# Kernel optimization log

Measured on AMD Instinct MI355X. Metric: run time of the kernel, lower is better.

Reference implementation:

```python
import jax, jax.numpy as jnp
import numpy as np

B, L, H, NH, DH = 2, 4096, 768, 12, 64
W_ = 128          # one-sided sliding window
NL = 2            # encoder layers
VOCAB, OUT, FF = 50265, 384, 3072
EPS = 1e-5


def _ln(x, s, b):
    m = jnp.mean(x, axis=-1, keepdims=True)
    v = jnp.mean((x - m) ** 2, axis=-1, keepdims=True)
    return (x - m) / jnp.sqrt(v + EPS) * s + b


def _attn(x, amask, Wq, bq, Wk, bk, Wv, bv, Wo, bo):
    # x: [B,L,H]; sliding-window attention (one-sided W_) + global token 0
    def heads(Wt, bt):
        return (x @ Wt + bt).reshape(B, L, NH, DH).transpose(0, 2, 1, 3)  # [B,NH,L,DH]
    q, k, v = heads(Wq, bq), heads(Wk, bk), heads(Wv, bv)
    scale = 1.0 / np.sqrt(DH).astype(np.float32)
    C = W_
    nC = L // C
    qc = q.reshape(B, NH, nC, C, DH)

    def blocks(t):  # gather [prev, self, next] key chunks -> [B,NH,nC,3C,DH]
        tc = t.reshape(B, NH, nC, C, DH)
        tp = jnp.pad(tc, ((0, 0), (0, 0), (1, 1), (0, 0), (0, 0)))
        return jnp.concatenate([tp[:, :, :-2], tp[:, :, 1:-1], tp[:, :, 2:]], axis=3)

    k3, v3 = blocks(k), blocks(v)
    s_loc = jnp.einsum('bhncd,bhnkd->bhnck', qc, k3) * scale  # [B,NH,nC,C,3C]

    pos_k = (jnp.arange(nC)[:, None] - 1) * C + jnp.arange(3 * C)[None, :]  # [nC,3C]
    pos_q = jnp.arange(nC)[:, None] * C + jnp.arange(C)[None, :]            # [nC,C]
    within = jnp.abs(pos_q[:, :, None] - pos_k[:, None, :]) <= W_           # [nC,C,3C]
    valid = (pos_k >= 0) & (pos_k < L) & (pos_k != 0)  # key 0 handled as global column
    mk = amask[:, jnp.clip(pos_k, 0, L - 1)] > 0        # [B,nC,3C]
    m = within[None, None] & valid[None, None, :, None, :] & mk[:, None, :, None, :]
    s_loc = jnp.where(m, s_loc, -1e9)

    # every token also attends to the global token 0
    s_g = jnp.einsum('bhld,bhd->bhl', q, k[:, :, 0]) * scale  # [B,NH,L]
    s = jnp.concatenate([s_loc.reshape(B, NH, L, 3 * C), s_g[..., None]], axis=-1)
    p = jax.nn.softmax(s, axis=-1)
    p_loc = p[..., :3 * C].reshape(B, NH, nC, C, 3 * C)
    out = jnp.einsum('bhnck,bhnkd->bhncd', p_loc, v3).reshape(B, NH, L, DH)
    out = out + p[..., -1:] * v[:, :, 0][:, :, None, :]

    # global token 0 attends to everything
    s0 = jnp.einsum('bhd,bhld->bhl', q[:, :, 0], k) * scale
    s0 = jnp.where(amask[:, None, :] > 0, s0, -1e9)
    o0 = jnp.einsum('bhl,bhld->bhd', jax.nn.softmax(s0, axis=-1), v)
    out = out.at[:, :, 0, :].set(o0)

    out = out.transpose(0, 2, 1, 3).reshape(B, L, H)
    return out @ Wo + bo


def setup_inputs() -> dict:
    key = jax.random.key(0)
    ks = jax.random.split(key, 16)
    p = lambda k_, sh: 0.02 * jax.random.normal(k_, sh, jnp.float32)
    return {
        'input_ids': jax.random.randint(ks[0], (B, L), 0, VOCAB, dtype=jnp.int32),
        'attention_mask': jnp.ones((B, L), jnp.int32),
        'word_emb': p(ks[1], (VOCAB, H)),
        'pos_emb': p(ks[2], (L, H)),
        'emb_ln_s': jnp.ones((H,), jnp.float32), 'emb_ln_b': jnp.zeros((H,), jnp.float32),
        'Wq': p(ks[3], (NL, H, H)), 'bq': jnp.zeros((NL, H), jnp.float32),
        'Wk': p(ks[4], (NL, H, H)), 'bk': jnp.zeros((NL, H), jnp.float32),
        'Wv': p(ks[5], (NL, H, H)), 'bv': jnp.zeros((NL, H), jnp.float32),
        'Wo': p(ks[6], (NL, H, H)), 'bo': jnp.zeros((NL, H), jnp.float32),
        'ln1_s': jnp.ones((NL, H), jnp.float32), 'ln1_b': jnp.zeros((NL, H), jnp.float32),
        'W1': p(ks[7], (NL, H, FF)), 'b1': jnp.zeros((NL, FF), jnp.float32),
        'W2': p(ks[8], (NL, FF, H)), 'b2': jnp.zeros((NL, H), jnp.float32),
        'ln2_s': jnp.ones((NL, H), jnp.float32), 'ln2_b': jnp.zeros((NL, H), jnp.float32),
        'Wfc': p(ks[9], (H, OUT)), 'bfc': jnp.zeros((OUT,), jnp.float32),
    }


def reference(input_ids, attention_mask, word_emb, pos_emb, emb_ln_s, emb_ln_b,
              Wq, bq, Wk, bk, Wv, bv, Wo, bo, ln1_s, ln1_b,
              W1, b1, W2, b2, ln2_s, ln2_b, Wfc, bfc):
    x = word_emb[input_ids] + pos_emb[None]
    x = _ln(x, emb_ln_s, emb_ln_b)
    for l in range(NL):
        a = _attn(x, attention_mask, Wq[l], bq[l], Wk[l], bk[l], Wv[l], bv[l], Wo[l], bo[l])
        x = _ln(x + a, ln1_s[l], ln1_b[l])
        h = jax.nn.gelu(x @ W1[l] + b1[l])
        x = _ln(x + h @ W2[l] + b2[l], ln2_s[l], ln2_b[l])
    v_dn = x @ Wfc + bfc           # [B,L,OUT]
    cls = v_dn[:, 0]               # fc(last_hidden[:,0]) == v_dn[:,0]
    return v_dn, cls
```

## Files before the change

kernel.cpp:

```cpp
#include <hip/hip_runtime.h>
#include <hip/hip_bf16.h>
#include <stdint.h>

#define L_SEQ 4096
#define H_DIM 768
#define N_HEADS 12
#define D_HEAD 64
#define N_CHUNK 32
#define CHUNK 128
#define FF_DIM 3072
#define OUT_DIM 384
#define BATCH 2
#define EPS_LN 1e-5f
#define M_ROWS (BATCH * L_SEQ)
#define QKV_LD (3 * H_DIM)
#define NSEG 16

typedef unsigned short u16;
typedef __bf16 bx8 __attribute__((ext_vector_type(8)));
typedef float fx4 __attribute__((ext_vector_type(4)));
typedef u16 ux8 __attribute__((ext_vector_type(8)));

__device__ __forceinline__ u16 f2bf(float f) {
  union { float f; unsigned u; } x; x.f = f;
  unsigned r = x.u + 0x7fffu + ((x.u >> 16) & 1u);
  return (u16)(r >> 16);
}
__device__ __forceinline__ float bf2f(u16 v) {
  union { unsigned u; float f; } x; x.u = ((unsigned)v) << 16;
  return x.f;
}

__device__ __forceinline__ void gload16(const void* g, void* l) {
  __builtin_amdgcn_global_load_lds((const __attribute__((address_space(1))) void*)g,
                                   (__attribute__((address_space(3))) void*)l, 16, 0, 0);
}

template<int OUT_BF16, int DO_GELU, int DO_CLS>
__global__ __launch_bounds__(256, 3)
void gemm_s(const u16* __restrict__ A, const u16* __restrict__ Bt,
            const float* __restrict__ bias,
            float* __restrict__ Cf, u16* __restrict__ Cb,
            float* __restrict__ cls,
            int N, int K)
{
  __shared__ __align__(16) u16 As[128 * 64];
  __shared__ __align__(16) u16 Bs[128 * 64];
  const int tid = threadIdx.x;
  const int lane = tid & 63, w = tid >> 6;
  const int c16 = lane & 15, g = lane >> 4;
  const int wr = w >> 1, wc = w & 1;

  const int nbn = N >> 7;
  int id = blockIdx.x;
  id = (id & 7) * (gridDim.x >> 3) + (id >> 3);
  const int bm = id / nbn, bn = id % nbn;

  const int srow = w * 8 + (lane >> 3);
  const int schunk = (lane & 7) ^ (lane >> 3);
  const u16* sA = A + (size_t)(bm * 128 + srow) * K + schunk * 8;
  const u16* sB = Bt + (size_t)(bn * 128 + srow) * K + schunk * 8;
  const int wdst = w * 512;

  fx4 acc[4][4] = {};

  for (int k0 = 0; k0 < K; k0 += 64) {
    #pragma unroll
    for (int i = 0; i < 4; i++) {
      gload16(sA + (size_t)(i * 32) * K + k0, &As[i * 2048 + wdst]);
      gload16(sB + (size_t)(i * 32) * K + k0, &Bs[i * 2048 + wdst]);
    }
    __syncthreads();
    #pragma unroll
    for (int h = 0; h < 2; h++) {
      bx8 af[4], bf[4];
      #pragma unroll
      for (int m = 0; m < 4; m++) {
        const int row = wr * 64 + m * 16 + c16;
        af[m] = *(const bx8*)&As[row * 64 + (((h << 2) + g) ^ (c16 & 7)) * 8];
      }
      #pragma unroll
      for (int n = 0; n < 4; n++) {
        const int row = wc * 64 + n * 16 + c16;
        bf[n] = *(const bx8*)&Bs[row * 64 + (((h << 2) + g) ^ (c16 & 7)) * 8];
      }
      #pragma unroll
      for (int m = 0; m < 4; m++)
        #pragma unroll
        for (int n = 0; n < 4; n++)
          acc[m][n] = __builtin_amdgcn_mfma_f32_16x16x32_bf16(af[m], bf[n], acc[m][n], 0, 0, 0);
    }
    __syncthreads();
  }

  const int row0 = bm * 128 + wr * 64 + g * 4;
  const int col0 = bn * 128 + wc * 64 + c16;
  #pragma unroll
  for (int n = 0; n < 4; n++) {
    const int col = col0 + n * 16;
    const float bb = bias[col];
    #pragma unroll
    for (int m = 0; m < 4; m++) {
      #pragma unroll
      for (int r = 0; r < 4; r++) {
        float y = acc[m][n][r] + bb;
        if (DO_GELU) {
          const float tt = y;
          y = 0.5f * tt * (1.0f + tanhf(0.7978845608f * (tt + 0.044715f * tt * tt * tt)));
        }
        const int row = row0 + m * 16 + r;
        const size_t idx = (size_t)row * N + col;
        if (OUT_BF16) Cb[idx] = f2bf(y);
        else Cf[idx] = y;
        if (DO_CLS) {
          if ((row & (L_SEQ - 1)) == 0)
            cls[(row >> 12) * OUT_DIM + col] = y;
        }
      }
    }
  }
}

#define V_STR 424

__global__ __launch_bounds__(512, 2)
void attn_local_kernel(const u16* __restrict__ qkv, const int* __restrict__ amask,
                       u16* __restrict__ attnout)
{
  __shared__ __align__(16) u16 Vlds[64 * V_STR];
  __shared__ __align__(16) u16 Plds[8 * 16 * V_STR];

  const int tid = threadIdx.x;
  const int lane = tid & 63, w = tid >> 6;
  const int c16 = lane & 15, g = lane >> 4;

  const int bh = blockIdx.x >> 5;
  const int n = blockIdx.x & 31;
  const int b = bh / N_HEADS, h = bh % N_HEADS;

  const u16* qkvb = qkv + (size_t)b * L_SEQ * QKV_LD + h * D_HEAD;
  const int chunk_lo = n * CHUNK - CHUNK;

  for (int idx = tid; idx < 416 * 8; idx += 512) {
    const int j = idx >> 3, d8 = (idx & 7) * 8;
    if (j >= 385) {
      #pragma unroll
      for (int i = 0; i < 8; i++) Vlds[(d8 + i) * V_STR + j] = 0;
    } else {
      int pos = (j == 384) ? 0 : chunk_lo + j;
      if (pos < 0 || pos >= L_SEQ) pos = 0;
      ux8 vv = *(const ux8*)(qkvb + (size_t)pos * QKV_LD + 2 * H_DIM + d8);
      #pragma unroll
      for (int i = 0; i < 8; i++) Vlds[(d8 + i) * V_STR + j] = vv[i];
    }
  }

  const int qrow = n * CHUNK + w * 16 + c16;
  const u16* qp = qkvb + (size_t)qrow * QKV_LD + g * 8;
  const bx8 aq0 = *(const bx8*)qp;
  const bx8 aq1 = *(const bx8*)(qp + 32);

  unsigned kvm = 0;
  #pragma unroll
  for (int kf = 0; kf < 24; kf++) {
    const int pos = chunk_lo + kf * 16 + c16;
    bool ok = (pos >= 1) && (pos < L_SEQ);
    if (ok) ok = (amask[b * L_SEQ + pos] > 0);
    kvm |= ((unsigned)ok) << kf;
  }

  fx4 s[26];
  #pragma unroll
  for (int kf = 0; kf < 25; kf++) {
    int pos = (kf == 24) ? 0 : chunk_lo + kf * 16 + c16;
    if (pos < 0 || pos >= L_SEQ) pos = 0;
    const u16* kp = qkvb + (size_t)pos * QKV_LD + H_DIM + g * 8;
    const bx8 b0 = *(const bx8*)kp;
    const bx8 b1 = *(const bx8*)(kp + 32);
    fx4 a = {};
    a = __builtin_amdgcn_mfma_f32_16x16x32_bf16(aq0, b0, a, 0, 0, 0);
    a = __builtin_amdgcn_mfma_f32_16x16x32_bf16(aq1, b1, a, 0, 0, 0);
    s[kf] = a;
  }

  const int cq = w * 16 + g * 4;
  float mx[4], sm[4];
  #pragma unroll
  for (int r = 0; r < 4; r++) mx[r] = -3.0e38f;
  #pragma unroll
  for (int kf = 0; kf < 25; kf++) {
    const int j = kf * 16 + c16;
    const bool kv = (kf < 24) ? (((kvm >> kf) & 1u) != 0) : (c16 == 0);
    #pragma unroll
    for (int r = 0; r < 4; r++) {
      const int c = cq + r;
      const bool keep = kv && (kf == 24 || (j >= c && j <= c + 256));
      const float val = keep ? s[kf][r] * 0.125f : -1.0e9f;
      s[kf][r] = val;
      mx[r] = fmaxf(mx[r], val);
    }
  }
  #pragma unroll
  for (int r = 0; r < 4; r++) {
    float m = mx[r];
    m = fmaxf(m, __shfl_xor(m, 1));
    m = fmaxf(m, __shfl_xor(m, 2));
    m = fmaxf(m, __shfl_xor(m, 4));
    m = fmaxf(m, __shfl_xor(m, 8));
    mx[r] = m;
    sm[r] = 0.f;
  }
  #pragma unroll
  for (int kf = 0; kf < 25; kf++)
    #pragma unroll
    for (int r = 0; r < 4; r++) {
      const float p = __expf(s[kf][r] - mx[r]);
      s[kf][r] = p;
      sm[r] += p;
    }
  float rinv[4];
  #pragma unroll
  for (int r = 0; r < 4; r++) {
    float t = sm[r];
    t += __shfl_xor(t, 1);
    t += __shfl_xor(t, 2);
    t += __shfl_xor(t, 4);
    t += __shfl_xor(t, 8);
    rinv[r] = 1.0f / t;
  }
  s[25] = (fx4){0.f, 0.f, 0.f, 0.f};

  u16* pb = Plds + (size_t)w * 16 * V_STR;
  #pragma unroll
  for (int kf = 0; kf < 26; kf++) {
    const int j = kf * 16 + c16;
    #pragma unroll
    for (int r = 0; r < 4; r++)
      pb[(g * 4 + r) * V_STR + j] = f2bf(s[kf][r]);
  }
  __syncthreads();

  fx4 o[4] = {};
  const u16* pr = Plds + (size_t)(w * 16 + c16) * V_STR + g * 8;
  #pragma unroll
  for (int kt = 0; kt < 13; kt++) {
    const bx8 pa = *(const bx8*)(pr + kt * 32);
    #pragma unroll
    for (int df = 0; df < 4; df++) {
      const bx8 vvf = *(const bx8*)&Vlds[(df * 16 + c16) * V_STR + kt * 32 + g * 8];
      o[df] = __builtin_amdgcn_mfma_f32_16x16x32_bf16(pa, vvf, o[df], 0, 0, 0);
    }
  }

  u16* ob = attnout + (size_t)b * L_SEQ * H_DIM + h * D_HEAD;
  const int posq = n * CHUNK + w * 16 + g * 4;
  #pragma unroll
  for (int df = 0; df < 4; df++)
    #pragma unroll
    for (int r = 0; r < 4; r++)
      ob[(size_t)(posq + r) * H_DIM + df * 16 + c16] = f2bf(o[df][r] * rinv[r]);
}

__global__ __launch_bounds__(256)
void attn_g_score(const u16* __restrict__ qkv, const int* __restrict__ amask,
                  float* __restrict__ sbuf, float* __restrict__ pmax)
{
  __shared__ float qs[D_HEAD];
  __shared__ float red[4];
  const int seg = blockIdx.x, bh = blockIdx.y;
  const int b = bh / N_HEADS, h = bh % N_HEADS;
  const u16* base = qkv + (size_t)b * L_SEQ * QKV_LD + h * D_HEAD;
  const int tid = threadIdx.x;

  if (tid < D_HEAD) qs[tid] = bf2f(base[tid]);
  __syncthreads();

  const int l = seg * 256 + tid;
  const ux8* kp = (const ux8*)(base + (size_t)l * QKV_LD + H_DIM);
  float dot = 0.f;
  #pragma unroll
  for (int i = 0; i < 8; i++) {
    const ux8 kv = kp[i];
    #pragma unroll
    for (int j = 0; j < 8; j++) dot += qs[i * 8 + j] * bf2f(kv[j]);
  }
  float sv = dot * 0.125f;
  if (amask[b * L_SEQ + l] == 0) sv = -1.0e9f;
  sbuf[(size_t)bh * L_SEQ + l] = sv;

  float m = sv;
  #pragma unroll
  for (int off = 32; off > 0; off >>= 1) m = fmaxf(m, __shfl_xor(m, off));
  if ((tid & 63) == 0) red[tid >> 6] = m;
  __syncthreads();
  if (tid == 0)
    pmax[bh * NSEG + seg] = fmaxf(fmaxf(red[0], red[1]), fmaxf(red[2], red[3]));
}

__global__ __launch_bounds__(256)
void attn_g_pv(const u16* __restrict__ qkv, const float* __restrict__ sbuf,
               const float* __restrict__ pmax, float* __restrict__ psum,
               float* __restrict__ po)
{
  __shared__ float es[256];
  __shared__ float red[4];
  const int seg = blockIdx.x, bh = blockIdx.y;
  const int b = bh / N_HEADS, h = bh % N_HEADS;
  const int tid = threadIdx.x;

  float M = -3.0e38f;
  #pragma unroll
  for (int i = 0; i < NSEG; i++) M = fmaxf(M, pmax[bh * NSEG + i]);

  const int l = seg * 256 + tid;
  const float e = __expf(sbuf[(size_t)bh * L_SEQ + l] - M);
  es[tid] = e;

  float t = e;
  #pragma unroll
  for (int off = 32; off > 0; off >>= 1) t += __shfl_xor(t, off);
  if ((tid & 63) == 0) red[tid >> 6] = t;
  __syncthreads();
  if (tid == 0) psum[bh * NSEG + seg] = red[0] + red[1] + red[2] + red[3];

  const int d = tid & 63, grp = tid >> 6;
  const u16* vb = qkv + (size_t)b * L_SEQ * QKV_LD + h * D_HEAD + 2 * H_DIM + d;
  float acc = 0.f;
  #pragma unroll 4
  for (int i = 0; i < 64; i++) {
    const int ll = seg * 256 + grp * 64 + i;
    acc += es[grp * 64 + i] * bf2f(vb[(size_t)ll * QKV_LD]);
  }
  po[(((size_t)bh * NSEG + seg) * 4 + grp) * D_HEAD + d] = acc;
}

__global__ __launch_bounds__(64)
void attn_g_combine(const float* __restrict__ psum, const float* __restrict__ po,
                    u16* __restrict__ attnout)
{
  const int bh = blockIdx.x;
  const int b = bh / N_HEADS, h = bh % N_HEADS;
  const int d = threadIdx.x;
  float S = 0.f;
  #pragma unroll
  for (int i = 0; i < NSEG; i++) S += psum[bh * NSEG + i];
  float acc = 0.f;
  #pragma unroll
  for (int i = 0; i < NSEG * 4; i++)
    acc += po[((size_t)bh * NSEG * 4 + i) * D_HEAD + d];
  attnout[(size_t)b * L_SEQ * H_DIM + h * D_HEAD + d] = f2bf(acc / S);
}

__device__ __forceinline__ void block_stats(float sum, float sq, float* red,
                                            float& mean, float& rstd)
{
  const int lane = threadIdx.x & 63, wv = threadIdx.x >> 6;
  #pragma unroll
  for (int off = 32; off > 0; off >>= 1) {
    sum += __shfl_xor(sum, off);
    sq  += __shfl_xor(sq, off);
  }
  if (lane == 0) { red[wv] = sum; red[4 + wv] = sq; }
  __syncthreads();
  sum = red[0] + red[1] + red[2] + red[3];
  sq  = red[4] + red[5] + red[6] + red[7];
  mean = sum * (1.0f / H_DIM);
  const float var = sq * (1.0f / H_DIM) - mean * mean;
  rstd = rsqrtf(var + EPS_LN);
}

__global__ __launch_bounds__(256)
void embed_ln_kernel(const int* __restrict__ ids, const float* __restrict__ wemb,
                     const float* __restrict__ pemb, const float* __restrict__ gam,
                     const float* __restrict__ bet, u16* __restrict__ xb)
{
  __shared__ float red[8];
  const int row = blockIdx.x, tid = threadIdx.x;
  const int l = row & (L_SEQ - 1);
  const int id = ids[row];
  float v[3]; float sum = 0.f, sq = 0.f;
  #pragma unroll
  for (int i = 0; i < 3; i++) {
    const int c = tid + i * 256;
    const float t = wemb[(size_t)id * H_DIM + c] + pemb[(size_t)l * H_DIM + c];
    v[i] = t; sum += t; sq += t * t;
  }
  float mean, rstd;
  block_stats(sum, sq, red, mean, rstd);
  #pragma unroll
  for (int i = 0; i < 3; i++) {
    const int c = tid + i * 256;
    const float y = (v[i] - mean) * rstd * gam[c] + bet[c];
    xb[(size_t)row * H_DIM + c] = f2bf(y);
  }
}

__global__ __launch_bounds__(256)
void add_ln_kernel(u16* xio, const u16* __restrict__ yin,
                   const float* __restrict__ gam, const float* __restrict__ bet)
{
  __shared__ float red[8];
  const int row = blockIdx.x, tid = threadIdx.x;
  float v[3]; float sum = 0.f, sq = 0.f;
  #pragma unroll
  for (int i = 0; i < 3; i++) {
    const int c = tid + i * 256;
    const float t = bf2f(xio[(size_t)row * H_DIM + c]) + bf2f(yin[(size_t)row * H_DIM + c]);
    v[i] = t; sum += t; sq += t * t;
  }
  float mean, rstd;
  block_stats(sum, sq, red, mean, rstd);
  #pragma unroll
  for (int i = 0; i < 3; i++) {
    const int c = tid + i * 256;
    const float y = (v[i] - mean) * rstd * gam[c] + bet[c];
    xio[(size_t)row * H_DIM + c] = f2bf(y);
  }
}

__global__ __launch_bounds__(256)
void prep_weights(const float* __restrict__ Wq, const float* __restrict__ Wk,
                  const float* __restrict__ Wv, const float* __restrict__ Wo,
                  const float* __restrict__ W1, const float* __restrict__ W2,
                  const float* __restrict__ Wfc,
                  const float* __restrict__ bq, const float* __restrict__ bk,
                  const float* __restrict__ bv,
                  u16* __restrict__ wqkvT, u16* __restrict__ woT,
                  u16* __restrict__ w1T, u16* __restrict__ w2T,
                  u16* __restrict__ wfcT, float* __restrict__ bqkv)
{
  const int t = blockIdx.x;
  const int tid = threadIdx.x;
  if (t >= 14112) {
    const int idx = t - 14112;
    const int l = idx / 9, j = idx % 9;
    const int i = j * 256 + tid;
    if (i < H_DIM)          bqkv[l * QKV_LD + i] = bq[l * H_DIM + i];
    else if (i < 2 * H_DIM) bqkv[l * QKV_LD + i] = bk[l * H_DIM + i - H_DIM];
    else if (i < 3 * H_DIM) bqkv[l * QKV_LD + i] = bv[l * H_DIM + i - 2 * H_DIM];
    return;
  }
  const float* src; u16* dst; int K, N, r;
  if (t < 13824) {
    const int l = t / 6912; r = t % 6912;
    if (r < 2304) {
      const int m = r / 576; r = r % 576; K = H_DIM; N = H_DIM;
      if (m == 0)      src = Wq + (size_t)l * H_DIM * H_DIM;
      else if (m == 1) src = Wk + (size_t)l * H_DIM * H_DIM;
      else if (m == 2) src = Wv + (size_t)l * H_DIM * H_DIM;
      else             src = Wo + (size_t)l * H_DIM * H_DIM;
      dst = (m < 3) ? wqkvT + (size_t)l * QKV_LD * H_DIM + (size_t)m * H_DIM * H_DIM
                    : woT + (size_t)l * H_DIM * H_DIM;
    } else if (r < 4608) {
      r -= 2304; K = H_DIM; N = FF_DIM;
      src = W1 + (size_t)l * H_DIM * FF_DIM;
      dst = w1T + (size_t)l * FF_DIM * H_DIM;
    } else {
      r -= 4608; K = FF_DIM; N = H_DIM;
      src = W2 + (size_t)l * FF_DIM * H_DIM;
      dst = w2T + (size_t)l * H_DIM * FF_DIM;
    }
  } else {
    r = t - 13824; K = H_DIM; N = OUT_DIM; src = Wfc; dst = wfcT;
  }
  const int ntn = N >> 5;
  const int k0 = (r / ntn) * 32, n0 = (r % ntn) * 32;
  __shared__ float tile[32][33];
  const int tx = tid & 31, ty = tid >> 5;
  #pragma unroll
  for (int i = 0; i < 32; i += 8)
    tile[ty + i][tx] = src[(size_t)(k0 + ty + i) * N + n0 + tx];
  __syncthreads();
  #pragma unroll
  for (int i = 0; i < 32; i += 8)
    dst[(size_t)(n0 + ty + i) * K + k0 + tx] = f2bf(tile[tx][ty + i]);
}

extern "C" void kernel_launch(void* const* d_in, const int* in_sizes, int n_in,
                              void* d_out, int out_size, void* d_ws, size_t ws_size,
                              hipStream_t stream)
{
  (void)in_sizes; (void)n_in; (void)out_size; (void)ws_size;
  const int*   ids   = (const int*)d_in[0];
  const int*   amask = (const int*)d_in[1];
  const float* wemb  = (const float*)d_in[2];
  const float* pemb  = (const float*)d_in[3];
  const float* elns  = (const float*)d_in[4];
  const float* elnb  = (const float*)d_in[5];
  const float* Wq    = (const float*)d_in[6];
  const float* bq    = (const float*)d_in[7];
  const float* Wk    = (const float*)d_in[8];
  const float* bk    = (const float*)d_in[9];
  const float* Wv    = (const float*)d_in[10];
  const float* bv    = (const float*)d_in[11];
  const float* Wo    = (const float*)d_in[12];
  const float* bo    = (const float*)d_in[13];
  const float* ln1s  = (const float*)d_in[14];
  const float* ln1b  = (const float*)d_in[15];
  const float* W1    = (const float*)d_in[16];
  const float* b1    = (const float*)d_in[17];
  const float* W2    = (const float*)d_in[18];
  const float* b2    = (const float*)d_in[19];
  const float* ln2s  = (const float*)d_in[20];
  const float* ln2b  = (const float*)d_in[21];
  const float* Wfc   = (const float*)d_in[22];
  const float* bfc   = (const float*)d_in[23];

  char* ws = (char*)d_ws;
  size_t off = 0;
  auto alloc = [&](size_t bytes) -> void* {
    void* p = ws + off;
    off += (bytes + 255) & ~(size_t)255;
    return p;
  };
  u16* xb     = (u16*)alloc((size_t)M_ROWS * H_DIM * 2);
  u16* projb  = (u16*)alloc((size_t)M_ROWS * H_DIM * 2);
  u16* big    = (u16*)alloc((size_t)M_ROWS * FF_DIM * 2);
  u16* attno  = (u16*)alloc((size_t)M_ROWS * H_DIM * 2);
  u16* wqkvT  = (u16*)alloc((size_t)2 * QKV_LD * H_DIM * 2);
  u16* woT    = (u16*)alloc((size_t)2 * H_DIM * H_DIM * 2);
  u16* w1T    = (u16*)alloc((size_t)2 * FF_DIM * H_DIM * 2);
  u16* w2T    = (u16*)alloc((size_t)2 * H_DIM * FF_DIM * 2);
  u16* wfcT   = (u16*)alloc((size_t)OUT_DIM * H_DIM * 2);
  float* bqkv = (float*)alloc(2 * QKV_LD * 4);
  float* gsc  = (float*)alloc((size_t)BATCH * N_HEADS * L_SEQ * 4);
  float* gpm  = (float*)alloc((size_t)BATCH * N_HEADS * NSEG * 4);
  float* gps  = (float*)alloc((size_t)BATCH * N_HEADS * NSEG * 4);
  float* gpo  = (float*)alloc((size_t)BATCH * N_HEADS * NSEG * 4 * D_HEAD * 4);

  u16* qkvb = big;
  u16* ff1  = big;

  prep_weights<<<14130, 256, 0, stream>>>(Wq, Wk, Wv, Wo, W1, W2, Wfc,
                                          bq, bk, bv,
                                          wqkvT, woT, w1T, w2T, wfcT, bqkv);
  embed_ln_kernel<<<M_ROWS, 256, 0, stream>>>(ids, wemb, pemb, elns, elnb, xb);

  for (int l = 0; l < 2; l++) {
    gemm_s<1, 0, 0><<<(M_ROWS / 128) * (QKV_LD / 128), 256, 0, stream>>>(
        xb, wqkvT + (size_t)l * QKV_LD * H_DIM, bqkv + l * QKV_LD,
        nullptr, qkvb, nullptr, QKV_LD, H_DIM);
    attn_local_kernel<<<BATCH * N_HEADS * N_CHUNK, 512, 0, stream>>>(qkvb, amask, attno);
    attn_g_score<<<dim3(NSEG, BATCH * N_HEADS), 256, 0, stream>>>(qkvb, amask, gsc, gpm);
    attn_g_pv<<<dim3(NSEG, BATCH * N_HEADS), 256, 0, stream>>>(qkvb, gsc, gpm, gps, gpo);
    attn_g_combine<<<BATCH * N_HEADS, 64, 0, stream>>>(gps, gpo, attno);
    gemm_s<1, 0, 0><<<(M_ROWS / 128) * (H_DIM / 128), 256, 0, stream>>>(
        attno, woT + (size_t)l * H_DIM * H_DIM, bo + l * H_DIM,
        nullptr, projb, nullptr, H_DIM, H_DIM);
    add_ln_kernel<<<M_ROWS, 256, 0, stream>>>(xb, projb, ln1s + l * H_DIM, ln1b + l * H_DIM);
    gemm_s<1, 1, 0><<<(M_ROWS / 128) * (FF_DIM / 128), 256, 0, stream>>>(
        xb, w1T + (size_t)l * FF_DIM * H_DIM, b1 + l * FF_DIM,
        nullptr, ff1, nullptr, FF_DIM, H_DIM);
    gemm_s<1, 0, 0><<<(M_ROWS / 128) * (H_DIM / 128), 256, 0, stream>>>(
        ff1, w2T + (size_t)l * H_DIM * FF_DIM, b2 + l * H_DIM,
        nullptr, projb, nullptr, H_DIM, FF_DIM);
    add_ln_kernel<<<M_ROWS, 256, 0, stream>>>(xb, projb, ln2s + l * H_DIM, ln2b + l * H_DIM);
  }

  float* vdn = (float*)d_out;
  float* cls = vdn + (size_t)BATCH * L_SEQ * OUT_DIM;
  gemm_s<0, 0, 1><<<(M_ROWS / 128) * (OUT_DIM / 128), 256, 0, stream>>>(
      xb, wfcT, bfc, vdn, nullptr, cls, OUT_DIM, H_DIM);
}
```

Baseline: 616.0 us.

## Swizzle LDS layout for V and P tiles and handle global token separately

Replaces the padded-stride LDS layout for the transposed V and probability tiles with an XOR-swizzled 384-wide layout to avoid bank conflicts. The global-token column is removed from the PV MFMA loop, which drops from 13 to 12 k-steps; its contribution is added in the epilogue using a lane-shuffled probability and the v[0] value. V staging changes to per-lane scalar gathers packed into 8-wide stores. This shrinks LDS use but trades vector global loads for strided scalar loads.

Result: no change. 621.5 us (+0.9%).

```diff
diff --git a/kernel.cpp b/kernel.cpp
--- a/kernel.cpp
+++ b/kernel.cpp
@@ -121,14 +121,14 @@
   }
 }
 
-#define V_STR 424
+#define KV_W 384
 
 __global__ __launch_bounds__(512, 2)
 void attn_local_kernel(const u16* __restrict__ qkv, const int* __restrict__ amask,
                        u16* __restrict__ attnout)
 {
-  __shared__ __align__(16) u16 Vlds[64 * V_STR];
-  __shared__ __align__(16) u16 Plds[8 * 16 * V_STR];
+  __shared__ __align__(16) u16 Vlds[64 * KV_W];
+  __shared__ __align__(16) u16 Plds[8 * 16 * KV_W];
 
   const int tid = threadIdx.x;
   const int lane = tid & 63, w = tid >> 6;
@@ -141,17 +141,20 @@
   const u16* qkvb = qkv + (size_t)b * L_SEQ * QKV_LD + h * D_HEAD;
   const int chunk_lo = n * CHUNK - CHUNK;
 
-  for (int idx = tid; idx < 416 * 8; idx += 512) {
-    const int j = idx >> 3, d8 = (idx & 7) * 8;
-    if (j >= 385) {
+  {
+    const int d = lane;
+    #pragma unroll
+    for (int it = 0; it < 6; it++) {
+      const int kb = it * 8 + w;
+      ux8 vals;
       #pragma unroll
-      for (int i = 0; i < 8; i++) Vlds[(d8 + i) * V_STR + j] = 0;
-    } else {
-      int pos = (j == 384) ? 0 : chunk_lo + j;
-      if (pos < 0 || pos >= L_SEQ) pos = 0;
-      ux8 vv = *(const ux8*)(qkvb + (size_t)pos * QKV_LD + 2 * H_DIM + d8);
-      #pragma unroll
-      for (int i = 0; i < 8; i++) Vlds[(d8 + i) * V_STR + j] = vv[i];
+      for (int j = 0; j < 8; j++) {
+        int pos = chunk_lo + kb * 8 + j;
+        if (pos < 0) pos = 0;
+        if (pos >= L_SEQ) pos = L_SEQ - 1;
+        vals[j] = qkvb[(size_t)pos * QKV_LD + 2 * H_DIM + d];
+      }
+      *(ux8*)&Vlds[d * KV_W + ((kb ^ (d & 7)) << 3)] = vals;
     }
   }
 
@@ -169,7 +172,7 @@
     kvm |= ((unsigned)ok) << kf;
   }
 
-  fx4 s[26];
+  fx4 s[25];
   #pragma unroll
   for (int kf = 0; kf < 25; kf++) {
     int pos = (kf == 24) ? 0 : chunk_lo + kf * 16 + c16;
@@ -228,26 +231,32 @@
     t += __shfl_xor(t, 8);
     rinv[r] = 1.0f / t;
   }
-  s[25] = (fx4){0.f, 0.f, 0.f, 0.f};
-
-  u16* pb = Plds + (size_t)w * 16 * V_STR;
-  #pragma unroll
-  for (int kf = 0; kf < 26; kf++) {
-    const int j = kf * 16 + c16;
-    #pragma unroll
-    for (int r = 0; r < 4; r++)
-      pb[(g * 4 + r) * V_STR + j] = f2bf(s[kf][r]);
+
+  float pg[4];
+  #pragma unroll
+  for (int r = 0; r < 4; r++) pg[r] = __shfl(s[24][r], g * 16);
+
+  u16* pb = Plds + (size_t)w * 16 * KV_W;
+  #pragma unroll
+  for (int kf = 0; kf < 24; kf++) {
+    #pragma unroll
+    for (int r = 0; r < 4; r++) {
+      const int rr = g * 4 + r;
+      const int j = kf * 16 + c16;
+      pb[rr * KV_W + (((j >> 3) ^ (rr & 7)) << 3) + (j & 7)] = f2bf(s[kf][r]);
+    }
   }
   __syncthreads();
 
   fx4 o[4] = {};
-  const u16* pr = Plds + (size_t)(w * 16 + c16) * V_STR + g * 8;
-  #pragma unroll
-  for (int kt = 0; kt < 13; kt++) {
-    const bx8 pa = *(const bx8*)(pr + kt * 32);
+  const int prow = (w * 16 + c16) * KV_W;
+  #pragma unroll
+  for (int kt = 0; kt < 12; kt++) {
+    const bx8 pa = *(const bx8*)&Plds[prow + (((kt * 4 + g) ^ (c16 & 7)) << 3)];
     #pragma unroll
     for (int df = 0; df < 4; df++) {
-      const bx8 vvf = *(const bx8*)&Vlds[(df * 16 + c16) * V_STR + kt * 32 + g * 8];
+      const int vrow = df * 16 + c16;
+      const bx8 vvf = *(const bx8*)&Vlds[vrow * KV_W + (((kt * 4 + g) ^ (c16 & 7)) << 3)];
       o[df] = __builtin_amdgcn_mfma_f32_16x16x32_bf16(pa, vvf, o[df], 0, 0, 0);
     }
   }
@@ -255,10 +264,13 @@
   u16* ob = attnout + (size_t)b * L_SEQ * H_DIM + h * D_HEAD;
   const int posq = n * CHUNK + w * 16 + g * 4;
   #pragma unroll
-  for (int df = 0; df < 4; df++)
+  for (int df = 0; df < 4; df++) {
+    const float v0f = bf2f(qkvb[2 * H_DIM + df * 16 + c16]);
     #pragma unroll
     for (int r = 0; r < 4; r++)
-      ob[(size_t)(posq + r) * H_DIM + df * 16 + c16] = f2bf(o[df][r] * rinv[r]);
+      ob[(size_t)(posq + r) * H_DIM + df * 16 + c16] =
+          f2bf((o[df][r] + pg[r] * v0f) * rinv[r]);
+  }
 }
 
 __global__ __launch_bounds__(256)
```
